# Kernel tuning notes

Hardware: AMD Instinct MI355X
Metric: run time of the kernel (lower is better)

The kernel has to match this reference:

```python
import jax, jax.numpy as jnp
import numpy as np

BATCH = 32768
DIM = 256
NUM_LATENTS = 4096
ENTROPY_WEIGHT = 0.1
VQ_BETA = 0.25
EPS = 1e-9


def _l2_normalize(v, axis=-1, eps=1e-12):
    # matches torch F.normalize(dim=-1)
    n = jnp.linalg.norm(v, axis=axis, keepdims=True)
    return v / jnp.maximum(n, eps)


def setup_inputs() -> dict:
    key = jax.random.key(0)
    kx, kc = jax.random.split(key)
    x = jax.random.normal(kx, (BATCH, DIM), dtype=jnp.float32)
    # codebook initialized uniform(-bound, bound) then row-normalized, as in __init__
    bound = (3.0 / DIM) ** 0.5
    cb = jax.random.uniform(kc, (NUM_LATENTS, DIM), dtype=jnp.float32,
                            minval=-bound, maxval=bound)
    codebook = _l2_normalize(cb)
    return {"x": x, "codebook": codebook}


def reference(x, codebook):
    # cosine-distance nearest-code lookup
    x_norm = _l2_normalize(x)                       # [B, D]
    cb_norm = _l2_normalize(codebook)               # [K, D]
    distance = -jnp.einsum('bd,kd->bk', x_norm, cb_norm)  # [B, K]
    # dropout p=0.0 -> identity
    indices = jnp.argmin(distance, axis=-1)         # [B] int
    z = codebook[indices]                           # [B, D] gather

    # straight-through estimator
    z_q = x + jax.lax.stop_gradient(z - x)

    commit_loss = jnp.mean((x - jax.lax.stop_gradient(z)) ** 2)
    q_loss = jnp.mean((z - jax.lax.stop_gradient(x)) ** 2)

    # entropy of codebook usage
    counts = jnp.bincount(indices, length=NUM_LATENTS).astype(jnp.float32)
    probs = counts / counts.sum()
    entropy = -jnp.sum(probs * jnp.log(jnp.clip(probs, EPS)))
    entropy_loss = -entropy

    vq_loss = q_loss + VQ_BETA * commit_loss + ENTROPY_WEIGHT * entropy_loss
    return (z_q, vq_loss, q_loss, commit_loss, entropy_loss, entropy, indices)
```

## Files before the change

### kernel.cpp

```cpp
#include <hip/hip_runtime.h>
#include <math.h>

#define BATCH 32768
#define DIM   256
#define NLAT  4096

typedef _Float16 f16x8 __attribute__((ext_vector_type(8)));
typedef float    f32x16 __attribute__((ext_vector_type(16)));

#define WS_CBH    0u
#define WS_CBINV  2097152u
#define WS_KEYS   2113536u
#define WS_HIST   4210688u

__device__ inline uint kenc(float v, int idx) {
  uint b = __float_as_uint(v);
  uint o = (b & 0x80000000u) ? ~b : (b ^ 0x80000000u);
  return (o & 0xFFFFF000u) | (uint)idx;
}
__device__ inline float kdec(uint key) {
  uint u = key & 0xFFFFF000u;
  uint bits = (u & 0x80000000u) ? (u ^ 0x80000000u) : ~u;
  return __uint_as_float(bits);
}

__global__ __launch_bounds__(256) void prep_kernel(
    const float* __restrict__ x, const float* __restrict__ cb,
    ushort* __restrict__ cbhf, float* __restrict__ cbinv,
    ushort* __restrict__ xh, int* __restrict__ hist) {
  int bid = blockIdx.x;
  if (bid < 1024) {
    int w = threadIdx.x >> 6, l = threadIdx.x & 63;
    int row = bid * 4 + w;
    const float4* cr = (const float4*)(cb + (size_t)row * DIM);
    float4 v = cr[l];
    float s = v.x * v.x + v.y * v.y + v.z * v.z + v.w * v.w;
    #pragma unroll
    for (int m = 32; m; m >>= 1) s += __shfl_xor(s, m, 64);
    float inv = 1.0f / fmaxf(sqrtf(s), 1e-12f);
    if (l == 0) cbinv[row] = inv;
    union { _Float16 h[4]; uint2 u; } pk;
    pk.h[0] = (_Float16)(v.x * inv);
    pk.h[1] = (_Float16)(v.y * inv);
    pk.h[2] = (_Float16)(v.z * inv);
    pk.h[3] = (_Float16)(v.w * inv);
    int t  = row >> 6, rf = (row >> 5) & 1, l31r = row & 31;
    int sl = l >> 2, lh2 = (l >> 1) & 1, half = l & 1;
    int lane = lh2 * 32 + l31r;
    ((uint2*)cbhf)[(((t * 16 + sl) * 2 + rf) << 7) + lane * 2 + half] = pk.u;
  } else if (bid < 5120) {
    int idx = (bid - 1024) * 256 + threadIdx.x;
    const float4* xs = (const float4*)x;
    float4 a = xs[idx * 2];
    float4 b = xs[idx * 2 + 1];
    union { _Float16 h[8]; uint4 u; } pk;
    pk.h[0] = (_Float16)a.x; pk.h[1] = (_Float16)a.y;
    pk.h[2] = (_Float16)a.z; pk.h[3] = (_Float16)a.w;
    pk.h[4] = (_Float16)b.x; pk.h[5] = (_Float16)b.y;
    pk.h[6] = (_Float16)b.z; pk.h[7] = (_Float16)b.w;
    ((uint4*)xh)[idx] = pk.u;
  } else {
    for (int k = threadIdx.x; k < NLAT; k += 256) hist[k] = 0;
  }
}

__global__ __launch_bounds__(256, 2) void vq_gemm_kernel(
    const ushort* __restrict__ xh, const char* __restrict__ cbhf,
    uint* __restrict__ keys) {
  const int tid = threadIdx.x;
  const int w = tid >> 6, l = tid & 63;
  const int l31 = l & 31, lh = l >> 5;
  const int bb = blockIdx.x >> 2, q = blockIdx.x & 3;
  const int wrow0 = bb * 256 + w * 64;
  const int cbase = q * 1024;

  f16x8 xf[16][2];
  #pragma unroll
  for (int fc = 0; fc < 2; ++fc) {
    const int row = wrow0 + fc * 32 + l31;
    const f16x8* xr = (const f16x8*)(xh + (size_t)row * DIM);
    #pragma unroll
    for (int s2 = 0; s2 < 16; ++s2) xf[s2][fc] = xr[s2 * 2 + lh];
  }

  const char* qbase = cbhf + (size_t)q * 524288 + (size_t)l * 16;
  f16x8 ring[4][2];
  #pragma unroll
  for (int s = 0; s < 3; ++s) {
    ring[s][0] = *(const f16x8*)(qbase + s * 2048);
    ring[s][1] = *(const f16x8*)(qbase + s * 2048 + 1024);
  }
  const char* pp = qbase + 6144;

  float tv1[2] = { -3e38f, -3e38f }, tv2[2] = { -3e38f, -3e38f },
        tv3[2] = { -3e38f, -3e38f };
  int   ti1[2] = { 0, 0 }, ti2[2] = { 0, 0 }, ti3[2] = { 0, 0 };

  #pragma unroll 1
  for (int t = 0; t < 16; ++t) {
    f32x16 acc[2][2];
    #pragma unroll
    for (int rf = 0; rf < 2; ++rf)
      #pragma unroll
      for (int fc = 0; fc < 2; ++fc)
        #pragma unroll
        for (int r = 0; r < 16; ++r) acc[rf][fc][r] = 0.f;

    #pragma unroll
    for (int sl = 0; sl < 16; ++sl) {
      ring[(sl + 3) & 3][0] = *(const f16x8*)(pp);
      ring[(sl + 3) & 3][1] = *(const f16x8*)(pp + 1024);
      pp += 2048;
      #pragma unroll
      for (int fc = 0; fc < 2; ++fc) {
        acc[0][fc] = __builtin_amdgcn_mfma_f32_32x32x16_f16(
            ring[sl & 3][0], xf[sl][fc], acc[0][fc], 0, 0, 0);
        acc[1][fc] = __builtin_amdgcn_mfma_f32_32x32x16_f16(
            ring[sl & 3][1], xf[sl][fc], acc[1][fc], 0, 0, 0);
      }
    }

    #pragma unroll
    for (int fc = 0; fc < 2; ++fc) {
      float mm[8];
      #pragma unroll
      for (int j = 0; j < 8; ++j)
        mm[j] = fmaxf(fmaxf(acc[0][fc][j], acc[0][fc][j + 8]),
                      fmaxf(acc[1][fc][j], acc[1][fc][j + 8]));
      float m0 = fmaxf(fmaxf(mm[0], mm[1]), fmaxf(mm[2], mm[3]));
      float m1 = fmaxf(fmaxf(mm[4], mm[5]), fmaxf(mm[6], mm[7]));
      float m = fmaxf(m0, m1);
      if (m > tv3[fc]) {
        #pragma unroll
        for (int rf = 0; rf < 2; ++rf)
          #pragma unroll
          for (int r = 0; r < 16; ++r) {
            float v = acc[rf][fc][r];
            if (v > tv3[fc]) {
              int code = cbase + t * 64 + rf * 32 + (r & 3) + 8 * (r >> 2) + 4 * lh;
              if (v > tv1[fc]) {
                tv3[fc] = tv2[fc]; ti3[fc] = ti2[fc];
                tv2[fc] = tv1[fc]; ti2[fc] = ti1[fc];
                tv1[fc] = v;       ti1[fc] = code;
              } else if (v > tv2[fc]) {
                tv3[fc] = tv2[fc]; ti3[fc] = ti2[fc];
                tv2[fc] = v;       ti2[fc] = code;
              } else {
                tv3[fc] = v;       ti3[fc] = code;
              }
            }
          }
      }
    }
  }

  #pragma unroll
  for (int fc = 0; fc < 2; ++fc) {
    float pv[6]; int pi[6];
    pv[0] = tv1[fc]; pv[1] = tv2[fc]; pv[2] = tv3[fc];
    pi[0] = ti1[fc]; pi[1] = ti2[fc]; pi[2] = ti3[fc];
    #pragma unroll
    for (int k = 0; k < 3; ++k) {
      pv[3 + k] = __shfl_xor(pv[k], 32, 64);
      pi[3 + k] = __shfl_xor(pi[k], 32, 64);
    }
    if (lh == 0) {
      float bv[4] = { -3e38f, -3e38f, -3e38f, -3e38f };
      int   bi[4] = { 0x7fffffff, 0x7fffffff, 0x7fffffff, 0x7fffffff };
      #pragma unroll
      for (int e = 0; e < 6; ++e) {
        float v = pv[e]; int ci = pi[e];
        #pragma unroll
        for (int k = 0; k < 4; ++k) {
          bool better = (v > bv[k]) || (v == bv[k] && ci < bi[k]);
          if (better) {
            float tvv = bv[k]; int tci = bi[k];
            bv[k] = v; bi[k] = ci;
            v = tvv; ci = tci;
          }
        }
      }
      int row = wrow0 + fc * 32 + l31;
      #pragma unroll
      for (int k = 0; k < 4; ++k)
        keys[row * 16 + q * 4 + k] = kenc(bv[k], bi[k] & (NLAT - 1));
    }
  }
}

__global__ __launch_bounds__(256) void rescore_kernel(
    const float* __restrict__ x, const float* __restrict__ cb,
    const float* __restrict__ cbinv, const uint* __restrict__ keys,
    float* __restrict__ zq, float* __restrict__ out_idx,
    int* __restrict__ hist, double* __restrict__ psse) {
  __shared__ float part[4];
  int tid = threadIdx.x, w = tid >> 6, l = tid & 63;
  int row = blockIdx.x * 4 + w;
  const float4* xr = (const float4*)(x + (size_t)row * DIM);
  float4 xv = xr[l];
  float s0 = xv.x * xv.x + xv.y * xv.y + xv.z * xv.z + xv.w * xv.w;
  #pragma unroll
  for (int m = 32; m; m >>= 1) s0 += __shfl_xor(s0, m, 64);
  float xnorm = sqrtf(s0);
  float xinv = 1.0f / fmaxf(xnorm, 1e-12f);

  uint key = keys[row * 16 + (l & 15)];
  uint kmax = key;
  #pragma unroll
  for (int m = 1; m < 16; m <<= 1) {
    uint o = __shfl_xor(kmax, m, 64);
    kmax = (o > kmax) ? o : kmax;
  }
  float dmax = kdec(kmax);
  float thr = dmax - 2.0f * (3e-3f * xnorm);
  bool inwin = (kdec(key) >= thr) && (l < 16);
  unsigned long long mask = __ballot(inwin);
  int besti;
  if (__popcll(mask) == 1) {
    besti = (int)(kmax & 0xFFFu);
  } else {
    float bestv = -3e38f; besti = 0x7fffffff;
    unsigned long long mm = mask;
    while (mm) {
      int b = __ffsll(mm) - 1; mm &= mm - 1;
      int ci = (int)(__shfl(key, b, 64) & 0xFFFu);
      float cbi = cbinv[ci];
      const float4* cr = (const float4*)(cb + (size_t)ci * DIM);
      float4 cv = cr[l];
      float d = (xv.x * xinv) * (cv.x * cbi) + (xv.y * xinv) * (cv.y * cbi)
              + (xv.z * xinv) * (cv.z * cbi) + (xv.w * xinv) * (cv.w * cbi);
      #pragma unroll
      for (int m = 32; m; m >>= 1) d += __shfl_xor(d, m, 64);
      bool better = (d > bestv) || (d == bestv && ci < besti);
      bestv = better ? d : bestv;
      besti = better ? ci : besti;
    }
  }

  float4 zv = ((const float4*)(cb + (size_t)besti * DIM))[l];
  float4 o;
  o.x = xv.x + (zv.x - xv.x); o.y = xv.y + (zv.y - xv.y);
  o.z = xv.z + (zv.z - xv.z); o.w = xv.w + (zv.w - xv.w);
  ((float4*)(zq + (size_t)row * DIM))[l] = o;
  float dx = xv.x - zv.x, dy = xv.y - zv.y, dz = xv.z - zv.z, dw = xv.w - zv.w;
  float s = dx * dx + dy * dy + dz * dz + dw * dw;
  #pragma unroll
  for (int m = 32; m; m >>= 1) s += __shfl_xor(s, m, 64);
  if (l == 0) part[w] = s;
  __syncthreads();
  if (tid == 0)
    psse[blockIdx.x] = (double)((part[0] + part[1]) + (part[2] + part[3]));
  if (l == 0) {
    atomicAdd(&hist[besti], 1);
    out_idx[row] = (float)besti;
  }
}

__global__ __launch_bounds__(256) void finalize_kernel(
    const int* __restrict__ hist, const double* __restrict__ psse,
    float* __restrict__ outs) {
  int tid = threadIdx.x;
  double e = 0.0, s = 0.0;
  for (int k = tid; k < NLAT; k += 256) {
    int c = hist[k];
    if (c > 0) {
      float p = (float)c * (1.0f / 32768.0f);
      e += (double)(p * logf(p));
    }
  }
  for (int k = tid; k < BATCH / 4; k += 256) s += psse[k];
  #pragma unroll
  for (int off = 32; off; off >>= 1) {
    e += __shfl_xor(e, off, 64);
    s += __shfl_xor(s, off, 64);
  }
  __shared__ double pe[4], ps[4];
  int w = tid >> 6, l = tid & 63;
  if (l == 0) { pe[w] = e; ps[w] = s; }
  __syncthreads();
  if (tid == 0) {
    double H = -((pe[0] + pe[1]) + (pe[2] + pe[3]));
    double sse = (ps[0] + ps[1]) + (ps[2] + ps[3]);
    double qv = sse * (1.0 / ((double)BATCH * (double)DIM));
    float qf = (float)qv;
    float Hf = (float)H;
    float ent_loss = -Hf;
    float vq = qf + 0.25f * qf + 0.1f * ent_loss;
    outs[0] = vq;
    outs[1] = qf;
    outs[2] = qf;
    outs[3] = ent_loss;
    outs[4] = Hf;
  }
}

extern "C" void kernel_launch(void* const* d_in, const int* in_sizes, int n_in,
                              void* d_out, int out_size, void* d_ws, size_t ws_size,
                              hipStream_t stream) {
  const float* x  = (const float*)d_in[0];
  const float* cb = (const float*)d_in[1];

  float* out     = (float*)d_out;
  float* zq      = out;
  float* scalars = out + (size_t)BATCH * DIM;
  float* oidx    = scalars + 5;

  char* wsb = (char*)d_ws;
  ushort* cbhf  = (ushort*)(wsb + WS_CBH);
  float*  cbinv = (float*)(wsb + WS_CBINV);
  uint*   keys  = (uint*)(wsb + WS_KEYS);
  int*    hist  = (int*)(wsb + WS_HIST);
  double* psse  = (double*)(wsb + WS_CBH);

  ushort* xh = (ushort*)d_out;

  prep_kernel<<<5121, 256, 0, stream>>>(x, cb, cbhf, cbinv, xh, hist);
  vq_gemm_kernel<<<512, 256, 0, stream>>>(xh, (const char*)cbhf, keys);
  rescore_kernel<<<BATCH / 4, 256, 0, stream>>>(x, cb, cbinv, keys,
                                                zq, oidx, hist, psse);
  finalize_kernel<<<1, 256, 0, stream>>>(hist, psse, scalars);
}
```

Baseline: 230.9 us.

## Shrink GEMM wave tile, pre-swizzle x fragments, use branchless packed-key top-3

Each wave now handles 32 rows instead of 64, and the grid doubles with a higher occupancy target, which cuts register pressure. x is written in an MFMA-fragment-swizzled layout so each lane can load it contiguously. The branchy float top-3 tracking becomes a branchless max/min network on packed uint keys. Accumulators start at 32.0 so the sums stay positive and raw float bits order correctly, which lets kdec drop the sign handling. In exchange, each codebook fragment is reused by half as many rows, so codebook load traffic per row doubles.

```diff
diff --git a/kernel.cpp b/kernel.cpp
--- a/kernel.cpp
+++ b/kernel.cpp
@@ -13,21 +13,14 @@
 #define WS_KEYS   2113536u
 #define WS_HIST   4210688u
 
-__device__ inline uint kenc(float v, int idx) {
-  uint b = __float_as_uint(v);
-  uint o = (b & 0x80000000u) ? ~b : (b ^ 0x80000000u);
-  return (o & 0xFFFFF000u) | (uint)idx;
-}
 __device__ inline float kdec(uint key) {
-  uint u = key & 0xFFFFF000u;
-  uint bits = (u & 0x80000000u) ? (u ^ 0x80000000u) : ~u;
-  return __uint_as_float(bits);
+  return __uint_as_float(key & 0xFFFFF000u);
 }
 
 __global__ __launch_bounds__(256) void prep_kernel(
     const float* __restrict__ x, const float* __restrict__ cb,
     ushort* __restrict__ cbhf, float* __restrict__ cbinv,
-    ushort* __restrict__ xh, int* __restrict__ hist) {
+    ushort* __restrict__ xhf, int* __restrict__ hist) {
   int bid = blockIdx.x;
   if (bid < 1024) {
     int w = threadIdx.x >> 6, l = threadIdx.x & 63;
@@ -58,133 +51,85 @@
     pk.h[2] = (_Float16)a.z; pk.h[3] = (_Float16)a.w;
     pk.h[4] = (_Float16)b.x; pk.h[5] = (_Float16)b.y;
     pk.h[6] = (_Float16)b.z; pk.h[7] = (_Float16)b.w;
-    ((uint4*)xh)[idx] = pk.u;
+    int row = idx >> 5, c = idx & 31;
+    int rowgrp = row >> 5, l31r = row & 31, sl = c >> 1, lhh = c & 1;
+    ((uint4*)xhf)[((size_t)rowgrp * 16 + sl) * 64 + lhh * 32 + l31r] = pk.u;
   } else {
     for (int k = threadIdx.x; k < NLAT; k += 256) hist[k] = 0;
   }
 }
 
-__global__ __launch_bounds__(256, 2) void vq_gemm_kernel(
-    const ushort* __restrict__ xh, const char* __restrict__ cbhf,
+__global__ __launch_bounds__(256, 4) void vq_gemm_kernel(
+    const char* __restrict__ xhf, const char* __restrict__ cbhf,
     uint* __restrict__ keys) {
   const int tid = threadIdx.x;
   const int w = tid >> 6, l = tid & 63;
   const int l31 = l & 31, lh = l >> 5;
   const int bb = blockIdx.x >> 2, q = blockIdx.x & 3;
-  const int wrow0 = bb * 256 + w * 64;
+  const int wrow0 = bb * 128 + w * 32;
   const int cbase = q * 1024;
-
-  f16x8 xf[16][2];
-  #pragma unroll
-  for (int fc = 0; fc < 2; ++fc) {
-    const int row = wrow0 + fc * 32 + l31;
-    const f16x8* xr = (const f16x8*)(xh + (size_t)row * DIM);
-    #pragma unroll
-    for (int s2 = 0; s2 < 16; ++s2) xf[s2][fc] = xr[s2 * 2 + lh];
-  }
+  const uint lh4u = (uint)(lh << 2);
+
+  const char* xb = xhf + ((size_t)(bb * 4 + w) * 1024 + l) * 16;
+  f16x8 xf[16];
+  #pragma unroll
+  for (int s2 = 0; s2 < 16; ++s2) xf[s2] = *(const f16x8*)(xb + s2 * 1024);
 
   const char* qbase = cbhf + (size_t)q * 524288 + (size_t)l * 16;
-  f16x8 ring[4][2];
-  #pragma unroll
-  for (int s = 0; s < 3; ++s) {
-    ring[s][0] = *(const f16x8*)(qbase + s * 2048);
-    ring[s][1] = *(const f16x8*)(qbase + s * 2048 + 1024);
-  }
-  const char* pp = qbase + 6144;
-
-  float tv1[2] = { -3e38f, -3e38f }, tv2[2] = { -3e38f, -3e38f },
-        tv3[2] = { -3e38f, -3e38f };
-  int   ti1[2] = { 0, 0 }, ti2[2] = { 0, 0 }, ti3[2] = { 0, 0 };
+  f16x8 ring[2][2];
+  ring[0][0] = *(const f16x8*)(qbase);
+  ring[0][1] = *(const f16x8*)(qbase + 1024);
+  const char* pp = qbase + 2048;
+
+  uint k1 = 0, k2 = 0, k3 = 0;
 
   #pragma unroll 1
   for (int t = 0; t < 16; ++t) {
-    f32x16 acc[2][2];
-    #pragma unroll
-    for (int rf = 0; rf < 2; ++rf)
+    f32x16 acc[2];
+    #pragma unroll
+    for (int r = 0; r < 16; ++r) { acc[0][r] = 32.0f; acc[1][r] = 32.0f; }
+
+    #pragma unroll
+    for (int sl = 0; sl < 16; ++sl) {
+      ring[(sl + 1) & 1][0] = *(const f16x8*)(pp);
+      ring[(sl + 1) & 1][1] = *(const f16x8*)(pp + 1024);
+      pp += 2048;
+      acc[0] = __builtin_amdgcn_mfma_f32_32x32x16_f16(
+          ring[sl & 1][0], xf[sl], acc[0], 0, 0, 0);
+      acc[1] = __builtin_amdgcn_mfma_f32_32x32x16_f16(
+          ring[sl & 1][1], xf[sl], acc[1], 0, 0, 0);
+    }
+
+    const uint scode = (uint)(cbase + t * 64);
+    #pragma unroll
+    for (int rf = 0; rf < 2; ++rf) {
       #pragma unroll
-      for (int fc = 0; fc < 2; ++fc)
-        #pragma unroll
-        for (int r = 0; r < 16; ++r) acc[rf][fc][r] = 0.f;
-
-    #pragma unroll
-    for (int sl = 0; sl < 16; ++sl) {
-      ring[(sl + 3) & 3][0] = *(const f16x8*)(pp);
-      ring[(sl + 3) & 3][1] = *(const f16x8*)(pp + 1024);
-      pp += 2048;
-      #pragma unroll
-      for (int fc = 0; fc < 2; ++fc) {
-        acc[0][fc] = __builtin_amdgcn_mfma_f32_32x32x16_f16(
-            ring[sl & 3][0], xf[sl][fc], acc[0][fc], 0, 0, 0);
-        acc[1][fc] = __builtin_amdgcn_mfma_f32_32x32x16_f16(
-            ring[sl & 3][1], xf[sl][fc], acc[1][fc], 0, 0, 0);
+      for (int r = 0; r < 16; ++r) {
+        const uint cr = (uint)(rf * 32 + (r & 3) + 8 * (r >> 2));
+        uint key = (__float_as_uint(acc[rf][r]) & 0xFFFFF000u)
+                 | scode | cr | lh4u;
+        uint m1 = max(k1, key), n1 = min(k1, key); k1 = m1;
+        uint m2 = max(k2, n1),  n2 = min(k2, n1);  k2 = m2;
+        k3 = max(k3, n2);
       }
     }
-
-    #pragma unroll
-    for (int fc = 0; fc < 2; ++fc) {
-      float mm[8];
-      #pragma unroll
-      for (int j = 0; j < 8; ++j)
-        mm[j] = fmaxf(fmaxf(acc[0][fc][j], acc[0][fc][j + 8]),
-                      fmaxf(acc[1][fc][j], acc[1][fc][j + 8]));
-      float m0 = fmaxf(fmaxf(mm[0], mm[1]), fmaxf(mm[2], mm[3]));
-      float m1 = fmaxf(fmaxf(mm[4], mm[5]), fmaxf(mm[6], mm[7]));
-      float m = fmaxf(m0, m1);
-      if (m > tv3[fc]) {
-        #pragma unroll
-        for (int rf = 0; rf < 2; ++rf)
-          #pragma unroll
-          for (int r = 0; r < 16; ++r) {
-            float v = acc[rf][fc][r];
-            if (v > tv3[fc]) {
-              int code = cbase + t * 64 + rf * 32 + (r & 3) + 8 * (r >> 2) + 4 * lh;
-              if (v > tv1[fc]) {
-                tv3[fc] = tv2[fc]; ti3[fc] = ti2[fc];
-                tv2[fc] = tv1[fc]; ti2[fc] = ti1[fc];
-                tv1[fc] = v;       ti1[fc] = code;
-              } else if (v > tv2[fc]) {
-                tv3[fc] = tv2[fc]; ti3[fc] = ti2[fc];
-                tv2[fc] = v;       ti2[fc] = code;
-              } else {
-                tv3[fc] = v;       ti3[fc] = code;
-              }
-            }
-          }
-      }
-    }
-  }
-
-  #pragma unroll
-  for (int fc = 0; fc < 2; ++fc) {
-    float pv[6]; int pi[6];
-    pv[0] = tv1[fc]; pv[1] = tv2[fc]; pv[2] = tv3[fc];
-    pi[0] = ti1[fc]; pi[1] = ti2[fc]; pi[2] = ti3[fc];
-    #pragma unroll
-    for (int k = 0; k < 3; ++k) {
-      pv[3 + k] = __shfl_xor(pv[k], 32, 64);
-      pi[3 + k] = __shfl_xor(pi[k], 32, 64);
-    }
-    if (lh == 0) {
-      float bv[4] = { -3e38f, -3e38f, -3e38f, -3e38f };
-      int   bi[4] = { 0x7fffffff, 0x7fffffff, 0x7fffffff, 0x7fffffff };
-      #pragma unroll
-      for (int e = 0; e < 6; ++e) {
-        float v = pv[e]; int ci = pi[e];
-        #pragma unroll
-        for (int k = 0; k < 4; ++k) {
-          bool better = (v > bv[k]) || (v == bv[k] && ci < bi[k]);
-          if (better) {
-            float tvv = bv[k]; int tci = bi[k];
-            bv[k] = v; bi[k] = ci;
-            v = tvv; ci = tci;
-          }
-        }
-      }
-      int row = wrow0 + fc * 32 + l31;
-      #pragma unroll
-      for (int k = 0; k < 4; ++k)
-        keys[row * 16 + q * 4 + k] = kenc(bv[k], bi[k] & (NLAT - 1));
-    }
+  }
+
+  uint o1 = __shfl_xor(k1, 32, 64);
+  uint o2 = __shfl_xor(k2, 32, 64);
+  uint o3 = __shfl_xor(k3, 32, 64);
+  uint k4 = 0;
+  #pragma unroll
+  for (int e = 0; e < 3; ++e) {
+    uint o = (e == 0) ? o1 : (e == 1) ? o2 : o3;
+    uint m = max(k1, o), n = min(k1, o); k1 = m;
+    m = max(k2, n); n = min(k2, n); k2 = m;
+    m = max(k3, n); n = min(k3, n); k3 = m;
+    k4 = max(k4, n);
+  }
+  if (lh == 0) {
+    uint4 kv; kv.x = k1; kv.y = k2; kv.z = k3; kv.w = k4;
+    *(uint4*)(keys + (size_t)(wrow0 + l31) * 16 + q * 4) = kv;
   }
 }
 
@@ -312,10 +257,11 @@
   int*    hist  = (int*)(wsb + WS_HIST);
   double* psse  = (double*)(wsb + WS_CBH);
 
-  ushort* xh = (ushort*)d_out;
-
-  prep_kernel<<<5121, 256, 0, stream>>>(x, cb, cbhf, cbinv, xh, hist);
-  vq_gemm_kernel<<<512, 256, 0, stream>>>(xh, (const char*)cbhf, keys);
+  ushort* xhf = (ushort*)d_out;
+
+  prep_kernel<<<5121, 256, 0, stream>>>(x, cb, cbhf, cbinv, xhf, hist);
+  vq_gemm_kernel<<<1024, 256, 0, stream>>>((const char*)xhf,
+                                           (const char*)cbhf, keys);
   rescore_kernel<<<BATCH / 4, 256, 0, stream>>>(x, cb, cbinv, keys,
                                                 zq, oidx, hist, psse);
   finalize_kernel<<<1, 256, 0, stream>>>(hist, psse, scalars);
```

Measured after the change: 222.3 us. 3.8% less time.
